# Kernel tuning notes

Measured on AMD Instinct MI355X. Metric: run time of the kernel, lower is better.

The kernel has to match this reference:

```python
import jax, jax.numpy as jnp
import numpy as np

H = 3072           # hidden_size
I = 8192           # intermediate_size
GS = 128           # quantization group size
B, S = 2, 2048


def dequant(qw, qz, scales, group_size=GS):
    """Group-wise int4 dequant: w = (q - zero) * scale.
    qw: [out, in] int8 nibbles in [0,16); qz: [out, in//g] int8; scales: [out, in//g] f32.
    """
    zp = jnp.repeat(qz.astype(jnp.float32), group_size, axis=1)
    sc = jnp.repeat(scales, group_size, axis=1)
    return (qw.astype(jnp.float32) - zp) * sc


def setup_inputs() -> dict:
    key = jax.random.key(0)
    ks = jax.random.split(key, 8)
    hidden_states = jax.random.normal(ks[0], (B, S, H), dtype=jnp.float32)
    # gate_up projection: [2*I, H], group-quantized along the input (H) dim
    gup_qw = jax.random.randint(ks[1], (2 * I, H), 0, 16, dtype=jnp.int8)
    gup_qz = jax.random.randint(ks[2], (2 * I, H // GS), 0, 16, dtype=jnp.int8)
    gup_scales = jax.random.uniform(ks[3], (2 * I, H // GS), dtype=jnp.float32, minval=0.005, maxval=0.02)
    # down projection: [H, I], group-quantized along the input (I) dim
    down_qw = jax.random.randint(ks[4], (H, I), 0, 16, dtype=jnp.int8)
    down_qz = jax.random.randint(ks[5], (H, I // GS), 0, 16, dtype=jnp.int8)
    down_scales = jax.random.uniform(ks[6], (H, I // GS), dtype=jnp.float32, minval=0.005, maxval=0.02)
    down_bias = jnp.zeros((H,), dtype=jnp.float32)
    return {
        "hidden_states": hidden_states,
        "gup_qw": gup_qw, "gup_qz": gup_qz, "gup_scales": gup_scales,
        "down_qw": down_qw, "down_qz": down_qz, "down_scales": down_scales,
        "down_bias": down_bias,
    }


def reference(hidden_states, gup_qw, gup_qz, gup_scales, down_qw, down_qz, down_scales, down_bias):
    W_gup = dequant(gup_qw, gup_qz, gup_scales)           # [2I, H]
    up_states = jnp.einsum('bsh,oh->bso', hidden_states, W_gup)  # [B,S,2I]
    gate, up = jnp.split(up_states, 2, axis=-1)
    act = jax.nn.silu(gate) * up                          # fused gate*act*up
    W_down = dequant(down_qw, down_qz, down_scales)       # [H, I]
    out = jnp.einsum('bsi,hi->bsh', act, W_down) + down_bias
    return out
```

## Files before the change

### kernel.cpp

```cpp
#include <hip/hip_runtime.h>


typedef float f32x4 __attribute__((ext_vector_type(4)));
typedef float f32x2 __attribute__((ext_vector_type(2)));
typedef int   i32x4 __attribute__((ext_vector_type(4)));

__device__ __forceinline__ void gload16(const void* g, void* l) {
  __builtin_amdgcn_global_load_lds(
      (const __attribute__((address_space(1))) void*)g,
      (__attribute__((address_space(3))) void*)l, 16, 0, 0);
}

__global__ __launch_bounds__(256) void quant_x(const float* __restrict__ x,
                                               signed char* __restrict__ Xq,
                                               float* __restrict__ Xs4) {
  int g    = blockIdx.x;
  int rq   = blockIdx.y;
  int w    = threadIdx.x >> 6;
  int lane = threadIdx.x & 63;
  int row  = rq * 4 + w;
  __shared__ float wmax[4];
  const float2 v = *(const float2*)(x + (size_t)row * 3072 + g * 128 + lane * 2);
  float m = fmaxf(fabsf(v.x), fabsf(v.y));
#pragma unroll
  for (int s = 1; s < 64; s <<= 1) m = fmaxf(m, __shfl_xor(m, s));
  if (lane == 0) wmax[w] = m;
  __syncthreads();
  float m4 = fmaxf(fmaxf(wmax[0], wmax[1]), fmaxf(wmax[2], wmax[3]));
  float inv = m4 > 0.f ? 127.f / m4 : 0.f;
  int qa = (int)rintf(v.x * inv);
  int qb = (int)rintf(v.y * inv);
  unsigned short pk = (unsigned short)((qa & 0xff) | ((qb & 0xff) << 8));
  *(unsigned short*)(Xq + (size_t)row * 3072 + g * 128 + lane * 2) = pk;
  if (threadIdx.x == 0) Xs4[g * 1024 + rq] = m4 * (1.f / 127.f);
}

template <int K>
__global__ __launch_bounds__(256) void requant_k(const int* __restrict__ qw,
                                                 const int* __restrict__ qz,
                                                 signed char* __restrict__ W) {
  constexpr int KG = K / 128;
  constexpr int perrow = K / 8;
  int idx = blockIdx.x * 256 + threadIdx.x;
  int row = idx / perrow;
  int c8  = idx - row * perrow;
  int k   = c8 << 3;
  int z   = qz[row * KG + (k >> 7)];
  const int4* q4 = (const int4*)(qw + (size_t)row * K + k);
  int4 qa = q4[0];
  int4 qb = q4[1];
  int b0 = ((qa.x - z) & 0xff) | (((qa.y - z) & 0xff) << 8) |
           (((qa.z - z) & 0xff) << 16) | (((qa.w - z) & 0xff) << 24);
  int b1 = ((qb.x - z) & 0xff) | (((qb.y - z) & 0xff) << 8) |
           (((qb.z - z) & 0xff) << 16) | (((qb.w - z) & 0xff) << 24);
  int2 o; o.x = b0; o.y = b1;
  *(int2*)(W + (size_t)row * K + k) = o;
}

__global__ __launch_bounds__(256) void transpose_sc(const float* __restrict__ in,
                                                    float* __restrict__ out,
                                                    int R, int G) {
  int idx = blockIdx.x * 256 + threadIdx.x;
  int r = idx / G;
  int g = idx - r * G;
  out[(size_t)g * R + r] = in[idx];
}


__global__ __launch_bounds__(256, 2) void gemm_gateup_i8(
    const signed char* __restrict__ Xq, const signed char* __restrict__ Wq,
    const float* __restrict__ Xs4,
    const float* __restrict__ GsT,
    signed char* __restrict__ act,
    float* __restrict__ As4) {
  const int K = 3072;
  const int bid = blockIdx.x;
  const int xcd = bid & 7;
  const int jb  = bid >> 3;
  const int n0  = ((xcd << 3) + (jb & 7)) * 128;
  const int m0  = (jb >> 3) * 128;
  __shared__ signed char lA[16384];
  __shared__ signed char lG[16384];
  __shared__ signed char lU[16384];
  __shared__ float rmax[2][128];
  __shared__ float rmax4[32];

  const int tid  = threadIdx.x;
  const int l    = tid & 63;
  const int quad = l >> 4;
  const int l16  = l & 15;
  const int wcI  = (tid >> 6) & 1;
  const int wr   = ((tid >> 6) >> 1) * 64;
  const int wc   = wcI * 64;

  f32x2 fg[4][4][2] = {};
  f32x2 fu[4][4][2] = {};

  int off[4];
#pragma unroll
  for (int jj = 0; jj < 4; ++jj) {
    int c   = tid + 256 * jj;
    int row = c >> 3;
    int log = (c & 7) ^ (row & 7);
    off[jj] = row * K + log * 16;
  }
  const signed char* baseA = Xq + (size_t)m0 * K;
  const signed char* baseG = Wq + (size_t)n0 * K;
  const signed char* baseU = Wq + (size_t)(8192 + n0) * K;

  int aoff[2][4], boff[2][4];
#pragma unroll
  for (int h = 0; h < 2; ++h) {
    int slot = h * 4 + quad;
#pragma unroll
    for (int i = 0; i < 4; ++i) {
      int ra = wr + i * 16 + l16;
      aoff[h][i] = ra * 128 + ((slot ^ (ra & 7)) * 16);
      int rb = wc + i * 16 + l16;
      boff[h][i] = rb * 128 + ((slot ^ (rb & 7)) * 16);
    }
  }
  const int qbase = (m0 >> 2) + (wr >> 2) + quad;

  for (int g = 0; g < 24; ++g) {
    const int kk = g << 7;
#pragma unroll
    for (int jj = 0; jj < 4; ++jj) {
      gload16(baseA + off[jj] + kk, lA + (tid + 256 * jj) * 16);
      gload16(baseG + off[jj] + kk, lG + (tid + 256 * jj) * 16);
      gload16(baseU + off[jj] + kk, lU + (tid + 256 * jj) * 16);
    }
    float sxq[4], sg[4], su[4];
#pragma unroll
    for (int i = 0; i < 4; ++i) sxq[i] = Xs4[g * 1024 + qbase + i * 4];
#pragma unroll
    for (int jj = 0; jj < 4; ++jj) {
      sg[jj] = GsT[g * 16384 + n0 + wc + jj * 16 + l16];
      su[jj] = GsT[g * 16384 + 8192 + n0 + wc + jj * 16 + l16];
    }
    __syncthreads();

    i32x4 a[4][2];
#pragma unroll
    for (int i = 0; i < 4; ++i) {
      a[i][0] = *(const i32x4*)(lA + aoff[0][i]);
      a[i][1] = *(const i32x4*)(lA + aoff[1][i]);
    }
#pragma unroll
    for (int jj = 0; jj < 4; ++jj) {
      i32x4 bg0 = *(const i32x4*)(lG + boff[0][jj]);
      i32x4 bg1 = *(const i32x4*)(lG + boff[1][jj]);
      i32x4 bu0 = *(const i32x4*)(lU + boff[0][jj]);
      i32x4 bu1 = *(const i32x4*)(lU + boff[1][jj]);
#pragma unroll
      for (int i = 0; i < 4; ++i) {
        i32x4 zero = {0, 0, 0, 0};
        i32x4 ig = __builtin_amdgcn_mfma_i32_16x16x64_i8(a[i][0], bg0, zero, 0, 0, 0);
        ig = __builtin_amdgcn_mfma_i32_16x16x64_i8(a[i][1], bg1, ig, 0, 0, 0);
        i32x4 iu = __builtin_amdgcn_mfma_i32_16x16x64_i8(a[i][0], bu0, zero, 0, 0, 0);
        iu = __builtin_amdgcn_mfma_i32_16x16x64_i8(a[i][1], bu1, iu, 0, 0, 0);
        float pgs = sxq[i] * sg[jj];
        float pus = sxq[i] * su[jj];
        f32x2 pg2 = {pgs, pgs};
        f32x2 pu2 = {pus, pus};
        f32x2 g01 = {(float)ig[0], (float)ig[1]};
        f32x2 g23 = {(float)ig[2], (float)ig[3]};
        f32x2 u01 = {(float)iu[0], (float)iu[1]};
        f32x2 u23 = {(float)iu[2], (float)iu[3]};
        fg[i][jj][0] = __builtin_elementwise_fma(g01, pg2, fg[i][jj][0]);
        fg[i][jj][1] = __builtin_elementwise_fma(g23, pg2, fg[i][jj][1]);
        fu[i][jj][0] = __builtin_elementwise_fma(u01, pu2, fu[i][jj][0]);
        fu[i][jj][1] = __builtin_elementwise_fma(u23, pu2, fu[i][jj][1]);
      }
    }
    __syncthreads();
  }

  float av[4][4][4];
#pragma unroll
  for (int i = 0; i < 4; ++i)
#pragma unroll
    for (int jj = 0; jj < 4; ++jj)
#pragma unroll
      for (int r = 0; r < 4; ++r) {
        float gv = fg[i][jj][r >> 1][r & 1];
        float uv = fu[i][jj][r >> 1][r & 1];
        av[i][jj][r] = (gv / (1.f + __expf(-gv))) * uv;
      }

#pragma unroll
  for (int i = 0; i < 4; ++i)
#pragma unroll
    for (int r = 0; r < 4; ++r) {
      float m = 0.f;
#pragma unroll
      for (int jj = 0; jj < 4; ++jj) m = fmaxf(m, fabsf(av[i][jj][r]));
      m = fmaxf(m, __shfl_xor(m, 1));
      m = fmaxf(m, __shfl_xor(m, 2));
      m = fmaxf(m, __shfl_xor(m, 4));
      m = fmaxf(m, __shfl_xor(m, 8));
      if (l16 == 0) rmax[wcI][wr + i * 16 + quad * 4 + r] = m;
    }
  __syncthreads();
  if (tid < 32) {
    float m = 0.f;
#pragma unroll
    for (int k = 0; k < 4; ++k)
      m = fmaxf(m, fmaxf(rmax[0][tid * 4 + k], rmax[1][tid * 4 + k]));
    rmax4[tid] = m;
    As4[(n0 >> 7) * 1024 + (m0 >> 2) + tid] = m * (1.f / 127.f);
  }
  __syncthreads();

#pragma unroll
  for (int i = 0; i < 4; ++i) {
    float mx = rmax4[(wr >> 2) + i * 4 + quad];
    float inv = mx > 0.f ? 127.f / mx : 0.f;
#pragma unroll
    for (int r = 0; r < 4; ++r) {
      int mrow = wr + i * 16 + quad * 4 + r;
#pragma unroll
      for (int jj = 0; jj < 4; ++jj) {
        int q = (int)rintf(av[i][jj][r] * inv);
        lA[mrow * 128 + wc + jj * 16 + l16] = (signed char)q;
      }
    }
  }
  __syncthreads();

#pragma unroll
  for (int t = 0; t < 4; ++t) {
    int c = tid + 256 * t;
    int row = c >> 3;
    int col = (c & 7) * 16;
    *(int4*)(act + (size_t)(m0 + row) * 8192 + n0 + col) = *(const int4*)(lA + row * 128 + col);
  }
}

__global__ __launch_bounds__(256, 2) void gemm_down_i8(
    const signed char* __restrict__ Aq, const signed char* __restrict__ Wq,
    const float* __restrict__ As4,
    const float* __restrict__ DsT,
    const float* __restrict__ bias,
    float* __restrict__ out) {
  const int K = 8192;
  const int bid = blockIdx.x;
  const int xcd = bid & 7;
  const int jb  = bid >> 3;
  const int jn  = jb % 12;
  const int jm  = jb / 12;
  const int n0  = (12 * (xcd & 1) + jn) * 128;
  const int m0  = (8 * (xcd >> 1) + jm) * 128;
  __shared__ signed char lA[16384];
  __shared__ signed char lB[16384];

  const int tid  = threadIdx.x;
  const int l    = tid & 63;
  const int quad = l >> 4;
  const int l16  = l & 15;
  const int wr   = ((tid >> 6) >> 1) * 64;
  const int wc   = ((tid >> 6) & 1) * 64;

  f32x2 fc[4][4][2] = {};

  int off[4];
#pragma unroll
  for (int jj = 0; jj < 4; ++jj) {
    int c   = tid + 256 * jj;
    int row = c >> 3;
    int log = (c & 7) ^ (row & 7);
    off[jj] = row * K + log * 16;
  }
  const signed char* baseA = Aq + (size_t)m0 * K;
  const signed char* baseB = Wq + (size_t)n0 * K;

  int aoff[2][4], boff[2][4];
#pragma unroll
  for (int h = 0; h < 2; ++h) {
    int slot = h * 4 + quad;
#pragma unroll
    for (int i = 0; i < 4; ++i) {
      int ra = wr + i * 16 + l16;
      aoff[h][i] = ra * 128 + ((slot ^ (ra & 7)) * 16);
      int rb = wc + i * 16 + l16;
      boff[h][i] = rb * 128 + ((slot ^ (rb & 7)) * 16);
    }
  }
  const int qbase = (m0 >> 2) + (wr >> 2) + quad;

  for (int g = 0; g < 64; ++g) {
    const int kk = g << 7;
#pragma unroll
    for (int jj = 0; jj < 4; ++jj) {
      gload16(baseA + off[jj] + kk, lA + (tid + 256 * jj) * 16);
      gload16(baseB + off[jj] + kk, lB + (tid + 256 * jj) * 16);
    }
    float sxq[4], sn[4];
#pragma unroll
    for (int i = 0; i < 4; ++i) sxq[i] = As4[g * 1024 + qbase + i * 4];
#pragma unroll
    for (int jj = 0; jj < 4; ++jj)
      sn[jj] = DsT[g * 3072 + n0 + wc + jj * 16 + l16];
    __syncthreads();

    i32x4 a[4][2];
#pragma unroll
    for (int i = 0; i < 4; ++i) {
      a[i][0] = *(const i32x4*)(lA + aoff[0][i]);
      a[i][1] = *(const i32x4*)(lA + aoff[1][i]);
    }
#pragma unroll
    for (int jj = 0; jj < 4; ++jj) {
      i32x4 b0 = *(const i32x4*)(lB + boff[0][jj]);
      i32x4 b1 = *(const i32x4*)(lB + boff[1][jj]);
#pragma unroll
      for (int i = 0; i < 4; ++i) {
        i32x4 zero = {0, 0, 0, 0};
        i32x4 ic = __builtin_amdgcn_mfma_i32_16x16x64_i8(a[i][0], b0, zero, 0, 0, 0);
        ic = __builtin_amdgcn_mfma_i32_16x16x64_i8(a[i][1], b1, ic, 0, 0, 0);
        float ps = sxq[i] * sn[jj];
        f32x2 p2 = {ps, ps};
        f32x2 c01 = {(float)ic[0], (float)ic[1]};
        f32x2 c23 = {(float)ic[2], (float)ic[3]};
        fc[i][jj][0] = __builtin_elementwise_fma(c01, p2, fc[i][jj][0]);
        fc[i][jj][1] = __builtin_elementwise_fma(c23, p2, fc[i][jj][1]);
      }
    }
    __syncthreads();
  }

  float bj[4];
#pragma unroll
  for (int jj = 0; jj < 4; ++jj) bj[jj] = bias[n0 + wc + jj * 16 + l16];

#pragma unroll
  for (int i = 0; i < 4; ++i)
#pragma unroll
    for (int jj = 0; jj < 4; ++jj)
#pragma unroll
      for (int r = 0; r < 4; ++r) {
        int m = m0 + wr + i * 16 + quad * 4 + r;
        int n = n0 + wc + jj * 16 + l16;
        out[(size_t)m * 3072 + n] = fc[i][jj][r >> 1][r & 1] + bj[jj];
      }
}

extern "C" void kernel_launch(void* const* d_in, const int* in_sizes, int n_in,
                              void* d_out, int out_size, void* d_ws, size_t ws_size,
                              hipStream_t stream) {
  const float* x        = (const float*)d_in[0];
  const int*   gup_qw   = (const int*)d_in[1];
  const int*   gup_qz   = (const int*)d_in[2];
  const float* gup_sc   = (const float*)d_in[3];
  const int*   down_qw  = (const int*)d_in[4];
  const int*   down_qz  = (const int*)d_in[5];
  const float* down_sc  = (const float*)d_in[6];
  const float* down_b   = (const float*)d_in[7];
  float* out = (float*)d_out;

  char* ws = (char*)d_ws;
  signed char* Xq    = (signed char*)(ws);
  signed char* Wgupq = (signed char*)(ws + 12582912);
  signed char* Wdnq  = (signed char*)(ws + 62914560);
  signed char* Actq  = (signed char*)(ws + 88080384);
  float* Xs4 = (float*)(ws + 121634816);
  float* GsT = (float*)(ws + 121733120);
  float* DsT = (float*)(ws + 123305984);
  float* As4 = (float*)(ws + 124092416);

  quant_x<<<dim3(24, 1024), 256, 0, stream>>>(x, Xq, Xs4);
  requant_k<3072><<<24576, 256, 0, stream>>>(gup_qw, gup_qz, Wgupq);
  requant_k<8192><<<12288, 256, 0, stream>>>(down_qw, down_qz, Wdnq);
  transpose_sc<<<1536, 256, 0, stream>>>(gup_sc, GsT, 16384, 24);
  transpose_sc<<<768, 256, 0, stream>>>(down_sc, DsT, 3072, 64);
  gemm_gateup_i8<<<2048, 256, 0, stream>>>(Xq, Wgupq, Xs4, GsT, Actq, As4);
  gemm_down_i8<<<768, 256, 0, stream>>>(Actq, Wdnq, As4, DsT, down_b, out);
}
```

Baseline: 806.9 us.

## Use 512-thread blocks, splitting gate and up across separate waves

Both int8 GEMM kernels move from 256 to 512 threads per block. In the gate/up kernel, half the waves accumulate gate and half accumulate up, which halves per-thread accumulator registers. The SiLU*up combine then goes through LDS in two phases with extra barriers. The down kernel splits its N tile across four column waves, which also halves accumulators per thread and should raise occupancy and latency hiding. The cost is more synchronization and an LDS round trip in the epilogue, with the same tile sizes and shared memory per block.

```diff
diff --git a/kernel.cpp b/kernel.cpp
--- a/kernel.cpp
+++ b/kernel.cpp
@@ -67,7 +67,7 @@
 }
 
 
-__global__ __launch_bounds__(256, 2) void gemm_gateup_i8(
+__global__ __launch_bounds__(512, 4) void gemm_gateup_i8(
     const signed char* __restrict__ Xq, const signed char* __restrict__ Wq,
     const float* __restrict__ Xs4,
     const float* __restrict__ GsT,
@@ -82,24 +82,25 @@
   __shared__ signed char lA[16384];
   __shared__ signed char lG[16384];
   __shared__ signed char lU[16384];
-  __shared__ float rmax[2][128];
-  __shared__ float rmax4[32];
+  __shared__ float rmaxp[2][64];
 
   const int tid  = threadIdx.x;
   const int l    = tid & 63;
   const int quad = l >> 4;
   const int l16  = l & 15;
-  const int wcI  = (tid >> 6) & 1;
-  const int wr   = ((tid >> 6) >> 1) * 64;
+  const int wave = tid >> 6;
+  const int isUp = wave >> 2;
+  const int w2   = wave & 3;
+  const int wcI  = w2 & 1;
+  const int wr   = (w2 >> 1) * 64;
   const int wc   = wcI * 64;
 
-  f32x2 fg[4][4][2] = {};
-  f32x2 fu[4][4][2] = {};
-
-  int off[4];
-#pragma unroll
-  for (int jj = 0; jj < 4; ++jj) {
-    int c   = tid + 256 * jj;
+  f32x2 f[4][4][2] = {};
+
+  int off[2];
+#pragma unroll
+  for (int jj = 0; jj < 2; ++jj) {
+    int c   = tid + 512 * jj;
     int row = c >> 3;
     int log = (c & 7) ^ (row & 7);
     off[jj] = row * K + log * 16;
@@ -107,6 +108,8 @@
   const signed char* baseA = Xq + (size_t)m0 * K;
   const signed char* baseG = Wq + (size_t)n0 * K;
   const signed char* baseU = Wq + (size_t)(8192 + n0) * K;
+  const signed char* lB    = isUp ? lU : lG;
+  const float* sWbase      = GsT + isUp * 8192 + n0 + wc;
 
   int aoff[2][4], boff[2][4];
 #pragma unroll
@@ -125,19 +128,16 @@
   for (int g = 0; g < 24; ++g) {
     const int kk = g << 7;
 #pragma unroll
-    for (int jj = 0; jj < 4; ++jj) {
-      gload16(baseA + off[jj] + kk, lA + (tid + 256 * jj) * 16);
-      gload16(baseG + off[jj] + kk, lG + (tid + 256 * jj) * 16);
-      gload16(baseU + off[jj] + kk, lU + (tid + 256 * jj) * 16);
-    }
-    float sxq[4], sg[4], su[4];
+    for (int jj = 0; jj < 2; ++jj) {
+      gload16(baseA + off[jj] + kk, lA + (tid + 512 * jj) * 16);
+      gload16(baseG + off[jj] + kk, lG + (tid + 512 * jj) * 16);
+      gload16(baseU + off[jj] + kk, lU + (tid + 512 * jj) * 16);
+    }
+    float sxq[4], sw[4];
 #pragma unroll
     for (int i = 0; i < 4; ++i) sxq[i] = Xs4[g * 1024 + qbase + i * 4];
 #pragma unroll
-    for (int jj = 0; jj < 4; ++jj) {
-      sg[jj] = GsT[g * 16384 + n0 + wc + jj * 16 + l16];
-      su[jj] = GsT[g * 16384 + 8192 + n0 + wc + jj * 16 + l16];
-    }
+    for (int jj = 0; jj < 4; ++jj) sw[jj] = sWbase[g * 16384 + jj * 16 + l16];
     __syncthreads();
 
     i32x4 a[4][2];
@@ -148,96 +148,97 @@
     }
 #pragma unroll
     for (int jj = 0; jj < 4; ++jj) {
-      i32x4 bg0 = *(const i32x4*)(lG + boff[0][jj]);
-      i32x4 bg1 = *(const i32x4*)(lG + boff[1][jj]);
-      i32x4 bu0 = *(const i32x4*)(lU + boff[0][jj]);
-      i32x4 bu1 = *(const i32x4*)(lU + boff[1][jj]);
+      i32x4 b0 = *(const i32x4*)(lB + boff[0][jj]);
+      i32x4 b1 = *(const i32x4*)(lB + boff[1][jj]);
 #pragma unroll
       for (int i = 0; i < 4; ++i) {
         i32x4 zero = {0, 0, 0, 0};
-        i32x4 ig = __builtin_amdgcn_mfma_i32_16x16x64_i8(a[i][0], bg0, zero, 0, 0, 0);
-        ig = __builtin_amdgcn_mfma_i32_16x16x64_i8(a[i][1], bg1, ig, 0, 0, 0);
-        i32x4 iu = __builtin_amdgcn_mfma_i32_16x16x64_i8(a[i][0], bu0, zero, 0, 0, 0);
-        iu = __builtin_amdgcn_mfma_i32_16x16x64_i8(a[i][1], bu1, iu, 0, 0, 0);
-        float pgs = sxq[i] * sg[jj];
-        float pus = sxq[i] * su[jj];
-        f32x2 pg2 = {pgs, pgs};
-        f32x2 pu2 = {pus, pus};
-        f32x2 g01 = {(float)ig[0], (float)ig[1]};
-        f32x2 g23 = {(float)ig[2], (float)ig[3]};
-        f32x2 u01 = {(float)iu[0], (float)iu[1]};
-        f32x2 u23 = {(float)iu[2], (float)iu[3]};
-        fg[i][jj][0] = __builtin_elementwise_fma(g01, pg2, fg[i][jj][0]);
-        fg[i][jj][1] = __builtin_elementwise_fma(g23, pg2, fg[i][jj][1]);
-        fu[i][jj][0] = __builtin_elementwise_fma(u01, pu2, fu[i][jj][0]);
-        fu[i][jj][1] = __builtin_elementwise_fma(u23, pu2, fu[i][jj][1]);
+        i32x4 ic = __builtin_amdgcn_mfma_i32_16x16x64_i8(a[i][0], b0, zero, 0, 0, 0);
+        ic = __builtin_amdgcn_mfma_i32_16x16x64_i8(a[i][1], b1, ic, 0, 0, 0);
+        float ps = sxq[i] * sw[jj];
+        f32x2 p2 = {ps, ps};
+        f32x2 c01 = {(float)ic[0], (float)ic[1]};
+        f32x2 c23 = {(float)ic[2], (float)ic[3]};
+        f[i][jj][0] = __builtin_elementwise_fma(c01, p2, f[i][jj][0]);
+        f[i][jj][1] = __builtin_elementwise_fma(c23, p2, f[i][jj][1]);
       }
     }
     __syncthreads();
   }
 
-  float av[4][4][4];
-#pragma unroll
-  for (int i = 0; i < 4; ++i)
-#pragma unroll
-    for (int jj = 0; jj < 4; ++jj)
-#pragma unroll
-      for (int r = 0; r < 4; ++r) {
-        float gv = fg[i][jj][r >> 1][r & 1];
-        float uv = fu[i][jj][r >> 1][r & 1];
-        av[i][jj][r] = (gv / (1.f + __expf(-gv))) * uv;
+  float* gb = (float*)(wcI ? lU : lG);
+#pragma unroll
+  for (int p = 0; p < 2; ++p) {
+    if (!isUp && (w2 >> 1) == p) {
+#pragma unroll
+      for (int i = 0; i < 4; ++i)
+#pragma unroll
+        for (int jj = 0; jj < 4; ++jj)
+#pragma unroll
+          for (int r = 0; r < 4; ++r)
+            gb[(i * 16 + quad * 4 + r) * 64 + jj * 16 + l16] = f[i][jj][r >> 1][r & 1];
+    }
+    __syncthreads();
+    if (isUp && (w2 >> 1) == p) {
+      float av[4][4][4];
+#pragma unroll
+      for (int i = 0; i < 4; ++i)
+#pragma unroll
+        for (int jj = 0; jj < 4; ++jj)
+#pragma unroll
+          for (int r = 0; r < 4; ++r) {
+            float gv = gb[(i * 16 + quad * 4 + r) * 64 + jj * 16 + l16];
+            float uv = f[i][jj][r >> 1][r & 1];
+            av[i][jj][r] = (gv / (1.f + __expf(-gv))) * uv;
+          }
+#pragma unroll
+      for (int i = 0; i < 4; ++i)
+#pragma unroll
+        for (int r = 0; r < 4; ++r) {
+          float m = 0.f;
+#pragma unroll
+          for (int jj = 0; jj < 4; ++jj) m = fmaxf(m, fabsf(av[i][jj][r]));
+          m = fmaxf(m, __shfl_xor(m, 1));
+          m = fmaxf(m, __shfl_xor(m, 2));
+          m = fmaxf(m, __shfl_xor(m, 4));
+          m = fmaxf(m, __shfl_xor(m, 8));
+          if (l16 == 0) rmaxp[wcI][i * 16 + quad * 4 + r] = m;
+        }
+      __syncthreads();
+#pragma unroll
+      for (int i = 0; i < 4; ++i) {
+        int lr0 = i * 16 + quad * 4;
+        float m4 = 0.f;
+#pragma unroll
+        for (int r = 0; r < 4; ++r)
+          m4 = fmaxf(m4, fmaxf(rmaxp[0][lr0 + r], rmaxp[1][lr0 + r]));
+        float inv = m4 > 0.f ? 127.f / m4 : 0.f;
+#pragma unroll
+        for (int r = 0; r < 4; ++r)
+#pragma unroll
+          for (int jj = 0; jj < 4; ++jj) {
+            int q = (int)rintf(av[i][jj][r] * inv);
+            lA[(p * 64 + lr0 + r) * 128 + wc + jj * 16 + l16] = (signed char)q;
+          }
+        if (l16 == 0 && wcI == 0)
+          As4[(n0 >> 7) * 1024 + ((m0 + p * 64 + lr0) >> 2)] = m4 * (1.f / 127.f);
       }
-
-#pragma unroll
-  for (int i = 0; i < 4; ++i)
-#pragma unroll
-    for (int r = 0; r < 4; ++r) {
-      float m = 0.f;
-#pragma unroll
-      for (int jj = 0; jj < 4; ++jj) m = fmaxf(m, fabsf(av[i][jj][r]));
-      m = fmaxf(m, __shfl_xor(m, 1));
-      m = fmaxf(m, __shfl_xor(m, 2));
-      m = fmaxf(m, __shfl_xor(m, 4));
-      m = fmaxf(m, __shfl_xor(m, 8));
-      if (l16 == 0) rmax[wcI][wr + i * 16 + quad * 4 + r] = m;
-    }
-  __syncthreads();
-  if (tid < 32) {
-    float m = 0.f;
-#pragma unroll
-    for (int k = 0; k < 4; ++k)
-      m = fmaxf(m, fmaxf(rmax[0][tid * 4 + k], rmax[1][tid * 4 + k]));
-    rmax4[tid] = m;
-    As4[(n0 >> 7) * 1024 + (m0 >> 2) + tid] = m * (1.f / 127.f);
-  }
-  __syncthreads();
-
-#pragma unroll
-  for (int i = 0; i < 4; ++i) {
-    float mx = rmax4[(wr >> 2) + i * 4 + quad];
-    float inv = mx > 0.f ? 127.f / mx : 0.f;
-#pragma unroll
-    for (int r = 0; r < 4; ++r) {
-      int mrow = wr + i * 16 + quad * 4 + r;
-#pragma unroll
-      for (int jj = 0; jj < 4; ++jj) {
-        int q = (int)rintf(av[i][jj][r] * inv);
-        lA[mrow * 128 + wc + jj * 16 + l16] = (signed char)q;
-      }
-    }
-  }
-  __syncthreads();
-
-#pragma unroll
-  for (int t = 0; t < 4; ++t) {
-    int c = tid + 256 * t;
+    } else {
+      __syncthreads();
+    }
+    __syncthreads();
+  }
+
+#pragma unroll
+  for (int t = 0; t < 2; ++t) {
+    int c = tid + 512 * t;
     int row = c >> 3;
     int col = (c & 7) * 16;
     *(int4*)(act + (size_t)(m0 + row) * 8192 + n0 + col) = *(const int4*)(lA + row * 128 + col);
   }
 }
 
-__global__ __launch_bounds__(256, 2) void gemm_down_i8(
+__global__ __launch_bounds__(512, 4) void gemm_down_i8(
     const signed char* __restrict__ Aq, const signed char* __restrict__ Wq,
     const float* __restrict__ As4,
     const float* __restrict__ DsT,
@@ -258,15 +259,16 @@
   const int l    = tid & 63;
   const int quad = l >> 4;
   const int l16  = l & 15;
-  const int wr   = ((tid >> 6) >> 1) * 64;
-  const int wc   = ((tid >> 6) & 1) * 64;
-
-  f32x2 fc[4][4][2] = {};
-
-  int off[4];
-#pragma unroll
-  for (int jj = 0; jj < 4; ++jj) {
-    int c   = tid + 256 * jj;
+  const int wave = tid >> 6;
+  const int wr   = (wave >> 2) * 64;
+  const int wc   = (wave & 3) * 32;
+
+  f32x2 fc[4][2][2] = {};
+
+  int off[2];
+#pragma unroll
+  for (int jj = 0; jj < 2; ++jj) {
+    int c   = tid + 512 * jj;
     int row = c >> 3;
     int log = (c & 7) ^ (row & 7);
     off[jj] = row * K + log * 16;
@@ -274,7 +276,7 @@
   const signed char* baseA = Aq + (size_t)m0 * K;
   const signed char* baseB = Wq + (size_t)n0 * K;
 
-  int aoff[2][4], boff[2][4];
+  int aoff[2][4], boff[2][2];
 #pragma unroll
   for (int h = 0; h < 2; ++h) {
     int slot = h * 4 + quad;
@@ -282,8 +284,11 @@
     for (int i = 0; i < 4; ++i) {
       int ra = wr + i * 16 + l16;
       aoff[h][i] = ra * 128 + ((slot ^ (ra & 7)) * 16);
-      int rb = wc + i * 16 + l16;
-      boff[h][i] = rb * 128 + ((slot ^ (rb & 7)) * 16);
+    }
+#pragma unroll
+    for (int jj = 0; jj < 2; ++jj) {
+      int rb = wc + jj * 16 + l16;
+      boff[h][jj] = rb * 128 + ((slot ^ (rb & 7)) * 16);
     }
   }
   const int qbase = (m0 >> 2) + (wr >> 2) + quad;
@@ -291,15 +296,15 @@
   for (int g = 0; g < 64; ++g) {
     const int kk = g << 7;
 #pragma unroll
-    for (int jj = 0; jj < 4; ++jj) {
-      gload16(baseA + off[jj] + kk, lA + (tid + 256 * jj) * 16);
-      gload16(baseB + off[jj] + kk, lB + (tid + 256 * jj) * 16);
-    }
-    float sxq[4], sn[4];
+    for (int jj = 0; jj < 2; ++jj) {
+      gload16(baseA + off[jj] + kk, lA + (tid + 512 * jj) * 16);
+      gload16(baseB + off[jj] + kk, lB + (tid + 512 * jj) * 16);
+    }
+    float sxq[4], sn[2];
 #pragma unroll
     for (int i = 0; i < 4; ++i) sxq[i] = As4[g * 1024 + qbase + i * 4];
 #pragma unroll
-    for (int jj = 0; jj < 4; ++jj)
+    for (int jj = 0; jj < 2; ++jj)
       sn[jj] = DsT[g * 3072 + n0 + wc + jj * 16 + l16];
     __syncthreads();
 
@@ -310,7 +315,7 @@
       a[i][1] = *(const i32x4*)(lA + aoff[1][i]);
     }
 #pragma unroll
-    for (int jj = 0; jj < 4; ++jj) {
+    for (int jj = 0; jj < 2; ++jj) {
       i32x4 b0 = *(const i32x4*)(lB + boff[0][jj]);
       i32x4 b1 = *(const i32x4*)(lB + boff[1][jj]);
 #pragma unroll
@@ -329,14 +334,14 @@
     __syncthreads();
   }
 
-  float bj[4];
-#pragma unroll
-  for (int jj = 0; jj < 4; ++jj) bj[jj] = bias[n0 + wc + jj * 16 + l16];
+  float bj[2];
+#pragma unroll
+  for (int jj = 0; jj < 2; ++jj) bj[jj] = bias[n0 + wc + jj * 16 + l16];
 
 #pragma unroll
   for (int i = 0; i < 4; ++i)
 #pragma unroll
-    for (int jj = 0; jj < 4; ++jj)
+    for (int jj = 0; jj < 2; ++jj)
 #pragma unroll
       for (int r = 0; r < 4; ++r) {
         int m = m0 + wr + i * 16 + quad * 4 + r;
@@ -373,6 +378,6 @@
   requant_k<8192><<<12288, 256, 0, stream>>>(down_qw, down_qz, Wdnq);
   transpose_sc<<<1536, 256, 0, stream>>>(gup_sc, GsT, 16384, 24);
   transpose_sc<<<768, 256, 0, stream>>>(down_sc, DsT, 3072, 64);
-  gemm_gateup_i8<<<2048, 256, 0, stream>>>(Xq, Wgupq, Xs4, GsT, Actq, As4);
-  gemm_down_i8<<<768, 256, 0, stream>>>(Actq, Wdnq, As4, DsT, down_b, out);
-}
+  gemm_gateup_i8<<<2048, 512, 0, stream>>>(Xq, Wgupq, Xs4, GsT, Actq, As4);
+  gemm_down_i8<<<768, 512, 0, stream>>>(Actq, Wdnq, As4, DsT, down_b, out);
+}
```

New measurement: 953.7 us. 1.18x slower.

## Halve gate-up N tile, requantize activations per 64 columns, doubling down-proj scale granularity

Applied to the files above, without the earlier changes.

The gate/up GEMM now uses 64-wide N tiles with 4096 blocks and a launch bound of 4 blocks per CU, reducing LDS and register use per block. The activation requant scale is now computed per 64 columns instead of 128. The down GEMM therefore splits each 128-wide K step into two 64-wide halves with separate activation scales, dropping the chained int32 accumulation across halves. This adds more per-half float conversions and FMAs in exchange for higher occupancy, finer activation quantization, and smaller per-block register state.

```diff
diff --git a/kernel.cpp b/kernel.cpp
--- a/kernel.cpp
+++ b/kernel.cpp
@@ -67,7 +67,7 @@
 }
 
 
-__global__ __launch_bounds__(256, 2) void gemm_gateup_i8(
+__global__ __launch_bounds__(256, 4) void gemm_gateup_i8(
     const signed char* __restrict__ Xq, const signed char* __restrict__ Wq,
     const float* __restrict__ Xs4,
     const float* __restrict__ GsT,
@@ -76,12 +76,12 @@
   const int K = 3072;
   const int bid = blockIdx.x;
   const int xcd = bid & 7;
-  const int jb  = bid >> 3;
-  const int n0  = ((xcd << 3) + (jb & 7)) * 128;
-  const int m0  = (jb >> 3) * 128;
+  const int j   = bid >> 3;
+  const int n0  = (xcd * 16 + (j & 15)) * 64;
+  const int m0  = (j >> 4) * 128;
   __shared__ signed char lA[16384];
-  __shared__ signed char lG[16384];
-  __shared__ signed char lU[16384];
+  __shared__ signed char lG[8192];
+  __shared__ signed char lU[8192];
   __shared__ float rmax[2][128];
   __shared__ float rmax4[32];
 
@@ -89,26 +89,32 @@
   const int l    = tid & 63;
   const int quad = l >> 4;
   const int l16  = l & 15;
-  const int wcI  = (tid >> 6) & 1;
-  const int wr   = ((tid >> 6) >> 1) * 64;
-  const int wc   = wcI * 64;
-
-  f32x2 fg[4][4][2] = {};
-  f32x2 fu[4][4][2] = {};
-
-  int off[4];
+  const int wave = tid >> 6;
+  const int wcI  = wave & 1;
+  const int wr   = (wave >> 1) * 64;
+  const int wc   = wcI * 32;
+
+  f32x2 fg[4][2][2] = {};
+  f32x2 fu[4][2][2] = {};
+
+  int offA[4], offW[2];
 #pragma unroll
   for (int jj = 0; jj < 4; ++jj) {
     int c   = tid + 256 * jj;
     int row = c >> 3;
-    int log = (c & 7) ^ (row & 7);
-    off[jj] = row * K + log * 16;
+    offA[jj] = row * K + (((c & 7) ^ (row & 7)) * 16);
+  }
+#pragma unroll
+  for (int jj = 0; jj < 2; ++jj) {
+    int c   = tid + 256 * jj;
+    int row = c >> 3;
+    offW[jj] = row * K + (((c & 7) ^ (row & 7)) * 16);
   }
   const signed char* baseA = Xq + (size_t)m0 * K;
   const signed char* baseG = Wq + (size_t)n0 * K;
   const signed char* baseU = Wq + (size_t)(8192 + n0) * K;
 
-  int aoff[2][4], boff[2][4];
+  int aoff[2][4], boff[2][2];
 #pragma unroll
   for (int h = 0; h < 2; ++h) {
     int slot = h * 4 + quad;
@@ -116,8 +122,11 @@
     for (int i = 0; i < 4; ++i) {
       int ra = wr + i * 16 + l16;
       aoff[h][i] = ra * 128 + ((slot ^ (ra & 7)) * 16);
-      int rb = wc + i * 16 + l16;
-      boff[h][i] = rb * 128 + ((slot ^ (rb & 7)) * 16);
+    }
+#pragma unroll
+    for (int jj = 0; jj < 2; ++jj) {
+      int rb = wc + jj * 16 + l16;
+      boff[h][jj] = rb * 128 + ((slot ^ (rb & 7)) * 16);
     }
   }
   const int qbase = (m0 >> 2) + (wr >> 2) + quad;
@@ -125,62 +134,60 @@
   for (int g = 0; g < 24; ++g) {
     const int kk = g << 7;
 #pragma unroll
-    for (int jj = 0; jj < 4; ++jj) {
-      gload16(baseA + off[jj] + kk, lA + (tid + 256 * jj) * 16);
-      gload16(baseG + off[jj] + kk, lG + (tid + 256 * jj) * 16);
-      gload16(baseU + off[jj] + kk, lU + (tid + 256 * jj) * 16);
-    }
-    float sxq[4], sg[4], su[4];
+    for (int jj = 0; jj < 4; ++jj)
+      gload16(baseA + offA[jj] + kk, lA + (tid + 256 * jj) * 16);
+#pragma unroll
+    for (int jj = 0; jj < 2; ++jj) {
+      gload16(baseG + offW[jj] + kk, lG + (tid + 256 * jj) * 16);
+      gload16(baseU + offW[jj] + kk, lU + (tid + 256 * jj) * 16);
+    }
+    float sxq[4], sg[2], su[2];
 #pragma unroll
     for (int i = 0; i < 4; ++i) sxq[i] = Xs4[g * 1024 + qbase + i * 4];
 #pragma unroll
-    for (int jj = 0; jj < 4; ++jj) {
+    for (int jj = 0; jj < 2; ++jj) {
       sg[jj] = GsT[g * 16384 + n0 + wc + jj * 16 + l16];
       su[jj] = GsT[g * 16384 + 8192 + n0 + wc + jj * 16 + l16];
     }
     __syncthreads();
 
-    i32x4 a[4][2];
-#pragma unroll
-    for (int i = 0; i < 4; ++i) {
-      a[i][0] = *(const i32x4*)(lA + aoff[0][i]);
-      a[i][1] = *(const i32x4*)(lA + aoff[1][i]);
-    }
-#pragma unroll
-    for (int jj = 0; jj < 4; ++jj) {
-      i32x4 bg0 = *(const i32x4*)(lG + boff[0][jj]);
-      i32x4 bg1 = *(const i32x4*)(lG + boff[1][jj]);
-      i32x4 bu0 = *(const i32x4*)(lU + boff[0][jj]);
-      i32x4 bu1 = *(const i32x4*)(lU + boff[1][jj]);
-#pragma unroll
-      for (int i = 0; i < 4; ++i) {
-        i32x4 zero = {0, 0, 0, 0};
-        i32x4 ig = __builtin_amdgcn_mfma_i32_16x16x64_i8(a[i][0], bg0, zero, 0, 0, 0);
-        ig = __builtin_amdgcn_mfma_i32_16x16x64_i8(a[i][1], bg1, ig, 0, 0, 0);
-        i32x4 iu = __builtin_amdgcn_mfma_i32_16x16x64_i8(a[i][0], bu0, zero, 0, 0, 0);
-        iu = __builtin_amdgcn_mfma_i32_16x16x64_i8(a[i][1], bu1, iu, 0, 0, 0);
-        float pgs = sxq[i] * sg[jj];
-        float pus = sxq[i] * su[jj];
-        f32x2 pg2 = {pgs, pgs};
-        f32x2 pu2 = {pus, pus};
-        f32x2 g01 = {(float)ig[0], (float)ig[1]};
-        f32x2 g23 = {(float)ig[2], (float)ig[3]};
-        f32x2 u01 = {(float)iu[0], (float)iu[1]};
-        f32x2 u23 = {(float)iu[2], (float)iu[3]};
-        fg[i][jj][0] = __builtin_elementwise_fma(g01, pg2, fg[i][jj][0]);
-        fg[i][jj][1] = __builtin_elementwise_fma(g23, pg2, fg[i][jj][1]);
-        fu[i][jj][0] = __builtin_elementwise_fma(u01, pu2, fu[i][jj][0]);
-        fu[i][jj][1] = __builtin_elementwise_fma(u23, pu2, fu[i][jj][1]);
+#pragma unroll
+    for (int h = 0; h < 2; ++h) {
+      i32x4 a[4];
+#pragma unroll
+      for (int i = 0; i < 4; ++i) a[i] = *(const i32x4*)(lA + aoff[h][i]);
+#pragma unroll
+      for (int jj = 0; jj < 2; ++jj) {
+        i32x4 bg = *(const i32x4*)(lG + boff[h][jj]);
+        i32x4 bu = *(const i32x4*)(lU + boff[h][jj]);
+#pragma unroll
+        for (int i = 0; i < 4; ++i) {
+          i32x4 zero = {0, 0, 0, 0};
+          i32x4 ig = __builtin_amdgcn_mfma_i32_16x16x64_i8(a[i], bg, zero, 0, 0, 0);
+          i32x4 iu = __builtin_amdgcn_mfma_i32_16x16x64_i8(a[i], bu, zero, 0, 0, 0);
+          float pgs = sxq[i] * sg[jj];
+          float pus = sxq[i] * su[jj];
+          f32x2 pg2 = {pgs, pgs};
+          f32x2 pu2 = {pus, pus};
+          f32x2 g01 = {(float)ig[0], (float)ig[1]};
+          f32x2 g23 = {(float)ig[2], (float)ig[3]};
+          f32x2 u01 = {(float)iu[0], (float)iu[1]};
+          f32x2 u23 = {(float)iu[2], (float)iu[3]};
+          fg[i][jj][0] = __builtin_elementwise_fma(g01, pg2, fg[i][jj][0]);
+          fg[i][jj][1] = __builtin_elementwise_fma(g23, pg2, fg[i][jj][1]);
+          fu[i][jj][0] = __builtin_elementwise_fma(u01, pu2, fu[i][jj][0]);
+          fu[i][jj][1] = __builtin_elementwise_fma(u23, pu2, fu[i][jj][1]);
+        }
       }
     }
     __syncthreads();
   }
 
-  float av[4][4][4];
+  float av[4][2][4];
 #pragma unroll
   for (int i = 0; i < 4; ++i)
 #pragma unroll
-    for (int jj = 0; jj < 4; ++jj)
+    for (int jj = 0; jj < 2; ++jj)
 #pragma unroll
       for (int r = 0; r < 4; ++r) {
         float gv = fg[i][jj][r >> 1][r & 1];
@@ -192,9 +199,7 @@
   for (int i = 0; i < 4; ++i)
 #pragma unroll
     for (int r = 0; r < 4; ++r) {
-      float m = 0.f;
-#pragma unroll
-      for (int jj = 0; jj < 4; ++jj) m = fmaxf(m, fabsf(av[i][jj][r]));
+      float m = fmaxf(fabsf(av[i][0][r]), fabsf(av[i][1][r]));
       m = fmaxf(m, __shfl_xor(m, 1));
       m = fmaxf(m, __shfl_xor(m, 2));
       m = fmaxf(m, __shfl_xor(m, 4));
@@ -203,41 +208,41 @@
     }
   __syncthreads();
   if (tid < 32) {
-    float m = 0.f;
+    float m4 = 0.f;
 #pragma unroll
     for (int k = 0; k < 4; ++k)
-      m = fmaxf(m, fmaxf(rmax[0][tid * 4 + k], rmax[1][tid * 4 + k]));
-    rmax4[tid] = m;
-    As4[(n0 >> 7) * 1024 + (m0 >> 2) + tid] = m * (1.f / 127.f);
+      m4 = fmaxf(m4, fmaxf(rmax[0][tid * 4 + k], rmax[1][tid * 4 + k]));
+    rmax4[tid] = m4;
+    As4[(n0 >> 6) * 1024 + (m0 >> 2) + tid] = m4 * (1.f / 127.f);
   }
   __syncthreads();
 
 #pragma unroll
   for (int i = 0; i < 4; ++i) {
-    float mx = rmax4[(wr >> 2) + i * 4 + quad];
-    float inv = mx > 0.f ? 127.f / mx : 0.f;
+    float mq = rmax4[(wr >> 2) + i * 4 + quad];
+    float inv = mq > 0.f ? 127.f / mq : 0.f;
 #pragma unroll
     for (int r = 0; r < 4; ++r) {
       int mrow = wr + i * 16 + quad * 4 + r;
 #pragma unroll
-      for (int jj = 0; jj < 4; ++jj) {
+      for (int jj = 0; jj < 2; ++jj) {
         int q = (int)rintf(av[i][jj][r] * inv);
-        lA[mrow * 128 + wc + jj * 16 + l16] = (signed char)q;
+        lA[mrow * 64 + wc + jj * 16 + l16] = (signed char)q;
       }
     }
   }
   __syncthreads();
 
 #pragma unroll
-  for (int t = 0; t < 4; ++t) {
+  for (int t = 0; t < 2; ++t) {
     int c = tid + 256 * t;
-    int row = c >> 3;
-    int col = (c & 7) * 16;
-    *(int4*)(act + (size_t)(m0 + row) * 8192 + n0 + col) = *(const int4*)(lA + row * 128 + col);
-  }
-}
-
-__global__ __launch_bounds__(256, 2) void gemm_down_i8(
+    int row = c >> 2;
+    int col = (c & 3) * 16;
+    *(int4*)(act + (size_t)(m0 + row) * 8192 + n0 + col) = *(const int4*)(lA + row * 64 + col);
+  }
+}
+
+__global__ __launch_bounds__(256, 4) void gemm_down_i8(
     const signed char* __restrict__ Aq, const signed char* __restrict__ Wq,
     const float* __restrict__ As4,
     const float* __restrict__ DsT,
@@ -258,8 +263,9 @@
   const int l    = tid & 63;
   const int quad = l >> 4;
   const int l16  = l & 15;
-  const int wr   = ((tid >> 6) >> 1) * 64;
-  const int wc   = ((tid >> 6) & 1) * 64;
+  const int wave = tid >> 6;
+  const int wr   = (wave >> 1) * 64;
+  const int wc   = (wave & 1) * 64;
 
   f32x2 fc[4][4][2] = {};
 
@@ -268,8 +274,7 @@
   for (int jj = 0; jj < 4; ++jj) {
     int c   = tid + 256 * jj;
     int row = c >> 3;
-    int log = (c & 7) ^ (row & 7);
-    off[jj] = row * K + log * 16;
+    off[jj] = row * K + (((c & 7) ^ (row & 7)) * 16);
   }
   const signed char* baseA = Aq + (size_t)m0 * K;
   const signed char* baseB = Wq + (size_t)n0 * K;
@@ -288,42 +293,43 @@
   }
   const int qbase = (m0 >> 2) + (wr >> 2) + quad;
 
-  for (int g = 0; g < 64; ++g) {
-    const int kk = g << 7;
+  for (int it = 0; it < 64; ++it) {
+    const int kk = it << 7;
 #pragma unroll
     for (int jj = 0; jj < 4; ++jj) {
       gload16(baseA + off[jj] + kk, lA + (tid + 256 * jj) * 16);
       gload16(baseB + off[jj] + kk, lB + (tid + 256 * jj) * 16);
     }
-    float sxq[4], sn[4];
-#pragma unroll
-    for (int i = 0; i < 4; ++i) sxq[i] = As4[g * 1024 + qbase + i * 4];
+    float sxq[2][4], sn[4];
+#pragma unroll
+    for (int h = 0; h < 2; ++h)
+#pragma unroll
+      for (int i = 0; i < 4; ++i)
+        sxq[h][i] = As4[(it * 2 + h) * 1024 + qbase + i * 4];
 #pragma unroll
     for (int jj = 0; jj < 4; ++jj)
-      sn[jj] = DsT[g * 3072 + n0 + wc + jj * 16 + l16];
+      sn[jj] = DsT[it * 3072 + n0 + wc + jj * 16 + l16];
     __syncthreads();
 
-    i32x4 a[4][2];
-#pragma unroll
-    for (int i = 0; i < 4; ++i) {
-      a[i][0] = *(const i32x4*)(lA + aoff[0][i]);
-      a[i][1] = *(const i32x4*)(lA + aoff[1][i]);
-    }
-#pragma unroll
-    for (int jj = 0; jj < 4; ++jj) {
-      i32x4 b0 = *(const i32x4*)(lB + boff[0][jj]);
-      i32x4 b1 = *(const i32x4*)(lB + boff[1][jj]);
-#pragma unroll
-      for (int i = 0; i < 4; ++i) {
-        i32x4 zero = {0, 0, 0, 0};
-        i32x4 ic = __builtin_amdgcn_mfma_i32_16x16x64_i8(a[i][0], b0, zero, 0, 0, 0);
-        ic = __builtin_amdgcn_mfma_i32_16x16x64_i8(a[i][1], b1, ic, 0, 0, 0);
-        float ps = sxq[i] * sn[jj];
-        f32x2 p2 = {ps, ps};
-        f32x2 c01 = {(float)ic[0], (float)ic[1]};
-        f32x2 c23 = {(float)ic[2], (float)ic[3]};
-        fc[i][jj][0] = __builtin_elementwise_fma(c01, p2, fc[i][jj][0]);
-        fc[i][jj][1] = __builtin_elementwise_fma(c23, p2, fc[i][jj][1]);
+#pragma unroll
+    for (int h = 0; h < 2; ++h) {
+      i32x4 a[4];
+#pragma unroll
+      for (int i = 0; i < 4; ++i) a[i] = *(const i32x4*)(lA + aoff[h][i]);
+#pragma unroll
+      for (int jj = 0; jj < 4; ++jj) {
+        i32x4 b = *(const i32x4*)(lB + boff[h][jj]);
+#pragma unroll
+        for (int i = 0; i < 4; ++i) {
+          i32x4 zero = {0, 0, 0, 0};
+          i32x4 ic = __builtin_amdgcn_mfma_i32_16x16x64_i8(a[i], b, zero, 0, 0, 0);
+          float ps = sxq[h][i] * sn[jj];
+          f32x2 p2 = {ps, ps};
+          f32x2 c01 = {(float)ic[0], (float)ic[1]};
+          f32x2 c23 = {(float)ic[2], (float)ic[3]};
+          fc[i][jj][0] = __builtin_elementwise_fma(c01, p2, fc[i][jj][0]);
+          fc[i][jj][1] = __builtin_elementwise_fma(c23, p2, fc[i][jj][1]);
+        }
       }
     }
     __syncthreads();
@@ -373,6 +379,6 @@
   requant_k<8192><<<12288, 256, 0, stream>>>(down_qw, down_qz, Wdnq);
   transpose_sc<<<1536, 256, 0, stream>>>(gup_sc, GsT, 16384, 24);
   transpose_sc<<<768, 256, 0, stream>>>(down_sc, DsT, 3072, 64);
-  gemm_gateup_i8<<<2048, 256, 0, stream>>>(Xq, Wgupq, Xs4, GsT, Actq, As4);
+  gemm_gateup_i8<<<4096, 256, 0, stream>>>(Xq, Wgupq, Xs4, GsT, Actq, As4);
   gemm_down_i8<<<768, 256, 0, stream>>>(Actq, Wdnq, As4, DsT, down_b, out);
 }
```

After: 1.716 ms. 2.13x slower.
